# Optimization experiments

Measured on AMD Instinct MI355X. Metric: run time of the kernel, lower is better.

The kernel has to match this reference:

```python
import jax, jax.numpy as jnp
import numpy as np

B, D, N_NEG, MAX_N = 4096, 256, 32768, 16
NEG_INF = float(jnp.finfo(jnp.float32).min)

def _l2norm(x):
    return x / jnp.linalg.norm(x, axis=-1, keepdims=True)

def setup_inputs() -> dict:
    key = jax.random.key(0)
    kq, kp, kn = jax.random.split(key, 3)
    q_emb = _l2norm(jax.random.normal(kq, (B, D), dtype=jnp.float32))
    p_emb = _l2norm(jax.random.normal(kp, (B, D), dtype=jnp.float32))
    n_emb = _l2norm(jax.random.normal(kn, (N_NEG, D), dtype=jnp.float32))
    # ragged counts in [0,16], mean 8, summing exactly to N_NEG
    rng = np.random.default_rng(0)
    d = rng.integers(0, 9, size=B // 2)
    counts = np.concatenate([8 + d, 8 - d])
    rng.shuffle(counts)
    n_counts = jnp.asarray(counts, dtype=jnp.int32)
    log_tau = jnp.log(jnp.asarray(0.07, dtype=jnp.float32))
    return {"q_emb": q_emb, "p_emb": p_emb, "n_emb": n_emb,
            "n_counts": n_counts, "log_tau": log_tau}

def reference(q_emb, p_emb, n_emb, n_counts, log_tau):
    Bq = q_emb.shape[0]
    tau = jnp.clip(jnp.exp(log_tau), 1e-4, 1.0)
    sim = (q_emb @ p_emb.T) / tau                      # [B, B]
    n_sim = (q_emb @ n_emb.T) / tau                    # [B, N]
    # vectorized ragged packing: query i's negatives live at
    # n_sim[i, offset[i] : offset[i]+cnt[i]]
    offsets = jnp.cumsum(n_counts) - n_counts          # [B]
    col = offsets[:, None] + jnp.arange(MAX_N)[None, :]
    valid = jnp.arange(MAX_N)[None, :] < n_counts[:, None]
    gathered = jnp.take_along_axis(n_sim, jnp.clip(col, 0, n_sim.shape[1] - 1), axis=1)
    neg_cols = jnp.where(valid, gathered, NEG_INF)     # [B, MAX_N]
    full = jnp.concatenate([sim, neg_cols], axis=1)    # [B, B+MAX_N]
    labels = jnp.arange(Bq)
    logp_q = jax.nn.log_softmax(full, axis=-1)
    loss_q = -jnp.mean(jnp.take_along_axis(logp_q, labels[:, None], axis=1))
    logp_p = jax.nn.log_softmax(sim.T, axis=-1)
    loss_p = -jnp.mean(jnp.take_along_axis(logp_p, labels[:, None], axis=1))
    return (loss_q + loss_p) / 2.0
```

## Files before the change

### kernel.cpp

```cpp
#include <hip/hip_runtime.h>
#include <math.h>

#define BQ 4096
#define DD 256
#define NNEG 32768

typedef __bf16 bf16x8 __attribute__((ext_vector_type(8)));
typedef float f32x4 __attribute__((ext_vector_type(4)));

typedef const __attribute__((address_space(1))) void GvPtr;
typedef __attribute__((address_space(3))) void LdsPtr;


__device__ __forceinline__ float get_inv_tau(const float* __restrict__ lt) {
  float tau = __expf(lt[0]);
  tau = fminf(fmaxf(tau, 1e-4f), 1.0f);
  return 1.0f / tau;
}

__device__ __forceinline__ unsigned int f2bf(float f) {
  unsigned int u = __float_as_uint(f);
  u += 0x7FFFu + ((u >> 16) & 1u);
  return u >> 16;
}

__global__ __launch_bounds__(256) void cvtscan_kernel(
    const float* __restrict__ q, const float* __restrict__ p,
    const int* __restrict__ counts,
    ushort* __restrict__ qb, ushort* __restrict__ pb,
    int* __restrict__ owner, float* __restrict__ rowcol ) {
  __shared__ int wtot[4];
  const int t = threadIdx.x;
  if (blockIdx.x < 1024) {
    const int i = blockIdx.x * 256 + t;
    const int half = (BQ * DD) / 8;
    const float* src = (i < half) ? q : p;
    ushort* dst = (i < half) ? qb : pb;
    const int idx = (i < half) ? i : (i - half);
    const float4 a = *reinterpret_cast<const float4*>(&src[idx * 8]);
    const float4 b = *reinterpret_cast<const float4*>(&src[idx * 8 + 4]);
    uint4 o;
    o.x = f2bf(a.x) | (f2bf(a.y) << 16);
    o.y = f2bf(a.z) | (f2bf(a.w) << 16);
    o.z = f2bf(b.x) | (f2bf(b.y) << 16);
    o.w = f2bf(b.z) | (f2bf(b.w) << 16);
    *reinterpret_cast<uint4*>(&dst[idx * 8]) = o;
    return;
  }
  const int wid = t >> 6, lane = t & 63;
  const float4 z = {0.f, 0.f, 0.f, 0.f};
#pragma unroll
  for (int i = 0; i < 8; ++i) reinterpret_cast<float4*>(rowcol)[t * 8 + i] = z;

  int cl[16];
  int s = 0;
#pragma unroll
  for (int i = 0; i < 4; ++i) {
    const int4 c = reinterpret_cast<const int4*>(counts)[t * 4 + i];
    cl[4 * i + 0] = c.x; cl[4 * i + 1] = c.y; cl[4 * i + 2] = c.z; cl[4 * i + 3] = c.w;
    s += c.x + c.y + c.z + c.w;
  }
  int x = s;
#pragma unroll
  for (int off = 1; off < 64; off <<= 1) {
    const int v = __shfl_up(x, off);
    if (lane >= off) x += v;
  }
  if (lane == 63) wtot[wid] = x;
  __syncthreads();
  int base = 0;
  for (int w = 0; w < wid; ++w) base += wtot[w];
  int running = base + x - s;
#pragma unroll
  for (int k = 0; k < 16; ++k) {
    const int qi = 16 * t + k;
    for (int e = 0; e < cl[k]; ++e) owner[running + e] = qi;
    running += cl[k];
  }
}

__global__ __launch_bounds__(256) void sim_kernel(
    const ushort* __restrict__ qb, const ushort* __restrict__ pb,
    const float* __restrict__ logtau,
    float* __restrict__ row_sum, float* __restrict__ col_sum,
    float* __restrict__ diag) {
  __shared__ ushort As[2][128 * 64];
  __shared__ ushort Bs[2][128 * 64];

  const int tid = threadIdx.x;
  const int lane = tid & 63;
  const int wv = tid >> 6;
  const int wr = wv >> 1, wc = wv & 1;
  const int lrow = lane >> 4;
  const int lcol = lane & 15;

  const int bid = (int)blockIdx.x;
  const int swz = (bid & 7) * 128 + (bid >> 3);
  const int bx = swz & 31, by = swz >> 5;
  const int brow = by * 128, bcol = bx * 128;

  const float inv_tau = get_inv_tau(logtau);

  const int sr = tid >> 3;
  const int sc = (tid & 7) * 8;

  f32x4 acc[4][4];
#pragma unroll
  for (int i = 0; i < 4; ++i)
#pragma unroll
    for (int j = 0; j < 4; ++j) acc[i][j] = (f32x4){0.f, 0.f, 0.f, 0.f};

#define STAGE(buf, k0)                                                          \
  {                                                                             \
    _Pragma("unroll")                                                           \
    for (int i = 0; i < 4; ++i) {                                               \
      const ushort* ga = qb + (size_t)(brow + i * 32 + sr) * DD + (k0) + sc;    \
      __builtin_amdgcn_global_load_lds((GvPtr*)ga,                              \
          (LdsPtr*)(&As[buf][0] + i * 2048 + tid * 8), 16, 0, 0);               \
    }                                                                           \
    _Pragma("unroll")                                                           \
    for (int i = 0; i < 4; ++i) {                                               \
      const ushort* gb = pb + (size_t)(bcol + i * 32 + sr) * DD + (k0) + sc;    \
      __builtin_amdgcn_global_load_lds((GvPtr*)gb,                              \
          (LdsPtr*)(&Bs[buf][0] + i * 2048 + tid * 8), 16, 0, 0);               \
    }                                                                           \
  }

  STAGE(0, 0);
  __syncthreads();

#pragma unroll
  for (int t = 0; t < 4; ++t) {
    if (t < 3) STAGE((t + 1) & 1, (t + 1) * 64);
    const ushort* lA = &As[t & 1][0];
    const ushort* lB = &Bs[t & 1][0];
#pragma unroll
    for (int sub = 0; sub < 2; ++sub) {
      const int kb = sub * 32 + lrow * 8;
      bf16x8 a[4], b[4];
#pragma unroll
      for (int m = 0; m < 4; ++m)
        a[m] = *reinterpret_cast<const bf16x8*>(lA + (wr * 64 + m * 16 + lcol) * 64 + kb);
#pragma unroll
      for (int n = 0; n < 4; ++n)
        b[n] = *reinterpret_cast<const bf16x8*>(lB + (wc * 64 + n * 16 + lcol) * 64 + kb);
#pragma unroll
      for (int m = 0; m < 4; ++m)
#pragma unroll
        for (int n = 0; n < 4; ++n)
          acc[m][n] = __builtin_amdgcn_mfma_f32_16x16x32_bf16(a[m], b[n], acc[m][n], 0, 0, 0);
    }
    __syncthreads();
  }
#undef STAGE

  const int arow0 = brow + wr * 64;
  const int bcol0 = bcol + wc * 64;
  float colp[4] = {0.f, 0.f, 0.f, 0.f};
#pragma unroll
  for (int mi = 0; mi < 4; ++mi) {
    float rowp[4] = {0.f, 0.f, 0.f, 0.f};
#pragma unroll
    for (int ni = 0; ni < 4; ++ni) {
      const f32x4 v = acc[mi][ni];
#pragma unroll
      for (int r = 0; r < 4; ++r) {
        const float sv = v[r] * inv_tau;
        const float e = __expf(sv);
        const int gr = arow0 + mi * 16 + lrow * 4 + r;
        const int gc = bcol0 + ni * 16 + lcol;
        if (gr == gc) diag[gr] = sv;
        rowp[r] += e;
        colp[ni] += e;
      }
    }
#pragma unroll
    for (int r = 0; r < 4; ++r) {
      float x = rowp[r];
      x += __shfl_xor(x, 1);
      x += __shfl_xor(x, 2);
      x += __shfl_xor(x, 4);
      x += __shfl_xor(x, 8);
      if (lcol == 0) atomicAdd(&row_sum[arow0 + mi * 16 + lrow * 4 + r], x);
    }
  }
#pragma unroll
  for (int ni = 0; ni < 4; ++ni) {
    float x = colp[ni];
    x += __shfl_xor(x, 16);
    x += __shfl_xor(x, 32);
    if (lrow == 0) atomicAdd(&col_sum[bcol0 + ni * 16 + lcol], x);
  }
}

__global__ __launch_bounds__(256) void neg_kernel(
    const float* __restrict__ q, const float* __restrict__ n_emb,
    const int* __restrict__ owner, const float* __restrict__ logtau,
    float* __restrict__ row_sum) {
  const int j = blockIdx.x * 64 + (threadIdx.x >> 2);
  const int sl = threadIdx.x & 3;
  const float inv_tau = get_inv_tau(logtau);
  const int ow = owner[j];
  const float4* nrow = reinterpret_cast<const float4*>(n_emb + (size_t)j * DD);
  const float4* qrow = reinterpret_cast<const float4*>(q + (size_t)ow * DD);
  float d = 0.f;
#pragma unroll
  for (int t = 0; t < 16; ++t) {
    const float4 nv = nrow[sl + 4 * t];
    const float4 qv = qrow[sl + 4 * t];
    d += qv.x * nv.x + qv.y * nv.y + qv.z * nv.z + qv.w * nv.w;
  }
  d += __shfl_xor(d, 1);
  d += __shfl_xor(d, 2);
  if (sl == 0) atomicAdd(&row_sum[ow], __expf(d * inv_tau));
}

__global__ __launch_bounds__(1024) void finalize_kernel(
    const float* __restrict__ row_sum, const float* __restrict__ col_sum,
    const float* __restrict__ diag, float* __restrict__ out) {
  __shared__ float ws[16];
  const int t = threadIdx.x;
  const int wid = t >> 6, lane = t & 63;
  const float4 r = reinterpret_cast<const float4*>(row_sum)[t];
  const float4 c = reinterpret_cast<const float4*>(col_sum)[t];
  const float4 d = reinterpret_cast<const float4*>(diag)[t];
  float v = __logf(r.x) + __logf(r.y) + __logf(r.z) + __logf(r.w)
          + __logf(c.x) + __logf(c.y) + __logf(c.z) + __logf(c.w)
          - 2.f * (d.x + d.y + d.z + d.w);
  v += __shfl_xor(v, 1);
  v += __shfl_xor(v, 2);
  v += __shfl_xor(v, 4);
  v += __shfl_xor(v, 8);
  v += __shfl_xor(v, 16);
  v += __shfl_xor(v, 32);
  if (lane == 0) ws[wid] = v;
  __syncthreads();
  if (wid == 0) {
    float x = (lane < 16) ? ws[lane] : 0.f;
    x += __shfl_xor(x, 1);
    x += __shfl_xor(x, 2);
    x += __shfl_xor(x, 4);
    x += __shfl_xor(x, 8);
    if (lane == 0) out[0] = x / (2.0f * BQ);
  }
}

extern "C" void kernel_launch(void* const* d_in, const int* in_sizes, int n_in,
                              void* d_out, int out_size, void* d_ws, size_t ws_size,
                              hipStream_t stream) {
  const float* q      = (const float*)d_in[0];
  const float* p      = (const float*)d_in[1];
  const float* n_emb  = (const float*)d_in[2];
  const int*   counts = (const int*)d_in[3];
  const float* logtau = (const float*)d_in[4];
  float* out = (float*)d_out;

  float* ws      = (float*)d_ws;
  float* row_sum = ws;
  float* col_sum = ws + BQ;
  float* diag    = ws + 2 * BQ;
  int*   owner   = (int*)(ws + 3 * BQ);
  ushort* qb     = (ushort*)(owner + NNEG);
  ushort* pb     = qb + (size_t)BQ * DD;

  cvtscan_kernel<<<1025, 256, 0, stream>>>(q, p, counts, qb, pb, owner, row_sum);
  neg_kernel<<<NNEG / 64, 256, 0, stream>>>(q, n_emb, owner, logtau, row_sum);
  sim_kernel<<<1024, 256, 0, stream>>>(qb, pb, logtau, row_sum, col_sum, diag);
  finalize_kernel<<<1, 1024, 0, stream>>>(row_sum, col_sum, diag, out);
}
```

Measured before the change: 138.3 us.

## Fuse negative-dot kernel into sim GEMM kernel and halve K tile

The separate negatives kernel is merged into the GEMM launch as an extra 1024 blocks. Each of these blocks handles 32 negatives, with 8 threads per negative dot product. The GEMM K-tile drops from 64 to 32 over 8 iterations, halving LDS use per block so more blocks can be resident. This removes one kernel launch and lets the memory-bound negative work overlap the MFMA work, at the cost of more barriers per GEMM tile.

Result: no change. 137.8 us (-0.3%).

```diff
diff --git a/kernel.cpp b/kernel.cpp
--- a/kernel.cpp
+++ b/kernel.cpp
@@ -79,30 +79,55 @@
   }
 }
 
-__global__ __launch_bounds__(256) void sim_kernel(
+__global__ __launch_bounds__(256) void simneg_kernel(
     const ushort* __restrict__ qb, const ushort* __restrict__ pb,
-    const float* __restrict__ logtau,
+    const float* __restrict__ q, const float* __restrict__ n_emb,
+    const int* __restrict__ owner, const float* __restrict__ logtau,
     float* __restrict__ row_sum, float* __restrict__ col_sum,
     float* __restrict__ diag) {
-  __shared__ ushort As[2][128 * 64];
-  __shared__ ushort Bs[2][128 * 64];
+  __shared__ ushort As[2][128 * 32];
+  __shared__ ushort Bs[2][128 * 32];
 
   const int tid = threadIdx.x;
+  const float inv_tau = get_inv_tau(logtau);
+  const int bid = (int)blockIdx.x;
+
+  if (bid >= 1024) {
+    const int j = (bid - 1024) * 32 + (tid >> 3);
+    const int sl = tid & 7;
+    const int ow = owner[j];
+    const float4* nrow = reinterpret_cast<const float4*>(n_emb + (size_t)j * DD);
+    const float4* qrow = reinterpret_cast<const float4*>(q + (size_t)ow * DD);
+    float d0 = 0.f, d1 = 0.f;
+#pragma unroll
+    for (int t = 0; t < 8; t += 2) {
+      const float4 n0 = nrow[sl + 8 * t];
+      const float4 q0 = qrow[sl + 8 * t];
+      const float4 n1 = nrow[sl + 8 * (t + 1)];
+      const float4 q1 = qrow[sl + 8 * (t + 1)];
+      d0 += q0.x * n0.x + q0.y * n0.y + q0.z * n0.z + q0.w * n0.w;
+      d1 += q1.x * n1.x + q1.y * n1.y + q1.z * n1.z + q1.w * n1.w;
+    }
+    float d = d0 + d1;
+    d += __shfl_xor(d, 1);
+    d += __shfl_xor(d, 2);
+    d += __shfl_xor(d, 4);
+    if (sl == 0) atomicAdd(&row_sum[ow], __expf(d * inv_tau));
+    return;
+  }
+
   const int lane = tid & 63;
   const int wv = tid >> 6;
   const int wr = wv >> 1, wc = wv & 1;
   const int lrow = lane >> 4;
   const int lcol = lane & 15;
 
-  const int bid = (int)blockIdx.x;
   const int swz = (bid & 7) * 128 + (bid >> 3);
   const int bx = swz & 31, by = swz >> 5;
   const int brow = by * 128, bcol = bx * 128;
 
-  const float inv_tau = get_inv_tau(logtau);
-
-  const int sr = tid >> 3;
-  const int sc = (tid & 7) * 8;
+  const int sr = tid >> 2;
+  const int sc = (tid & 3) * 8;
 
   f32x4 acc[4][4];
 #pragma unroll
@@ -113,14 +138,11 @@
 #define STAGE(buf, k0)                                                          \
   {                                                                             \
     _Pragma("unroll")                                                           \
-    for (int i = 0; i < 4; ++i) {                                               \
-      const ushort* ga = qb + (size_t)(brow + i * 32 + sr) * DD + (k0) + sc;    \
+    for (int i = 0; i < 2; ++i) {                                               \
+      const ushort* ga = qb + (size_t)(brow + i * 64 + sr) * DD + (k0) + sc;    \
       __builtin_amdgcn_global_load_lds((GvPtr*)ga,                              \
           (LdsPtr*)(&As[buf][0] + i * 2048 + tid * 8), 16, 0, 0);               \
-    }                                                                           \
-    _Pragma("unroll")                                                           \
-    for (int i = 0; i < 4; ++i) {                                               \
-      const ushort* gb = pb + (size_t)(bcol + i * 32 + sr) * DD + (k0) + sc;    \
+      const ushort* gb = pb + (size_t)(bcol + i * 64 + sr) * DD + (k0) + sc;    \
       __builtin_amdgcn_global_load_lds((GvPtr*)gb,                              \
           (LdsPtr*)(&Bs[buf][0] + i * 2048 + tid * 8), 16, 0, 0);               \
     }                                                                           \
@@ -130,26 +152,22 @@
   __syncthreads();
 
 #pragma unroll
-  for (int t = 0; t < 4; ++t) {
-    if (t < 3) STAGE((t + 1) & 1, (t + 1) * 64);
+  for (int t = 0; t < 8; ++t) {
+    if (t < 7) STAGE((t + 1) & 1, (t + 1) * 32);
     const ushort* lA = &As[t & 1][0];
     const ushort* lB = &Bs[t & 1][0];
-#pragma unroll
-    for (int sub = 0; sub < 2; ++sub) {
-      const int kb = sub * 32 + lrow * 8;
-      bf16x8 a[4], b[4];
-#pragma unroll
-      for (int m = 0; m < 4; ++m)
-        a[m] = *reinterpret_cast<const bf16x8*>(lA + (wr * 64 + m * 16 + lcol) * 64 + kb);
+    bf16x8 a[4], b[4];
+#pragma unroll
+    for (int m = 0; m < 4; ++m)
+      a[m] = *reinterpret_cast<const bf16x8*>(lA + (wr * 64 + m * 16 + lcol) * 32 + lrow * 8);
+#pragma unroll
+    for (int n = 0; n < 4; ++n)
+      b[n] = *reinterpret_cast<const bf16x8*>(lB + (wc * 64 + n * 16 + lcol) * 32 + lrow * 8);
+#pragma unroll
+    for (int m = 0; m < 4; ++m)
 #pragma unroll
       for (int n = 0; n < 4; ++n)
-        b[n] = *reinterpret_cast<const bf16x8*>(lB + (wc * 64 + n * 16 + lcol) * 64 + kb);
-#pragma unroll
-      for (int m = 0; m < 4; ++m)
-#pragma unroll
-        for (int n = 0; n < 4; ++n)
-          acc[m][n] = __builtin_amdgcn_mfma_f32_16x16x32_bf16(a[m], b[n], acc[m][n], 0, 0, 0);
-    }
+        acc[m][n] = __builtin_amdgcn_mfma_f32_16x16x32_bf16(a[m], b[n], acc[m][n], 0, 0, 0);
     __syncthreads();
   }
 #undef STAGE
@@ -191,28 +209,6 @@
     x += __shfl_xor(x, 32);
     if (lrow == 0) atomicAdd(&col_sum[bcol0 + ni * 16 + lcol], x);
   }
-}
-
-__global__ __launch_bounds__(256) void neg_kernel(
-    const float* __restrict__ q, const float* __restrict__ n_emb,
-    const int* __restrict__ owner, const float* __restrict__ logtau,
-    float* __restrict__ row_sum) {
-  const int j = blockIdx.x * 64 + (threadIdx.x >> 2);
-  const int sl = threadIdx.x & 3;
-  const float inv_tau = get_inv_tau(logtau);
-  const int ow = owner[j];
-  const float4* nrow = reinterpret_cast<const float4*>(n_emb + (size_t)j * DD);
-  const float4* qrow = reinterpret_cast<const float4*>(q + (size_t)ow * DD);
-  float d = 0.f;
-#pragma unroll
-  for (int t = 0; t < 16; ++t) {
-    const float4 nv = nrow[sl + 4 * t];
-    const float4 qv = qrow[sl + 4 * t];
-    d += qv.x * nv.x + qv.y * nv.y + qv.z * nv.z + qv.w * nv.w;
-  }
-  d += __shfl_xor(d, 1);
-  d += __shfl_xor(d, 2);
-  if (sl == 0) atomicAdd(&row_sum[ow], __expf(d * inv_tau));
 }
 
 __global__ __launch_bounds__(1024) void finalize_kernel(
@@ -264,7 +260,7 @@
   ushort* pb     = qb + (size_t)BQ * DD;
 
   cvtscan_kernel<<<1025, 256, 0, stream>>>(q, p, counts, qb, pb, owner, row_sum);
-  neg_kernel<<<NNEG / 64, 256, 0, stream>>>(q, n_emb, owner, logtau, row_sum);
-  sim_kernel<<<1024, 256, 0, stream>>>(qb, pb, logtau, row_sum, col_sum, diag);
+  simneg_kernel<<<2048, 256, 0, stream>>>(qb, pb, q, n_emb, owner, logtau,
+                                          row_sum, col_sum, diag);
   finalize_kernel<<<1, 1024, 0, stream>>>(row_sum, col_sum, diag, out);
 }
```
